# Kernel optimization log

Hardware: AMD Instinct MI355X
Metric: run time of the kernel (lower is better)

## Reference

```python
import jax, jax.numpy as jnp
import numpy as np
from functools import partial

T, B, IN, H = 512, 32, 1024, 1024
NUM_LAYERS = 2
SLOPE, OFFSET = 0.2, 0.5
FORGET_GATE_BIAS = 1.0
W_SCALE = 1.0 / np.sqrt(H)  # mimics reset_parameters uniform(-1/sqrt(H), 1/sqrt(H)) scale


def setup_inputs() -> dict:
    key = jax.random.key(0)
    ks = jax.random.split(key, 12)
    x = jax.random.normal(ks[0], (T, B, IN), dtype=jnp.float32)
    h0 = jax.random.normal(ks[1], (NUM_LAYERS, B, H), dtype=jnp.float32)
    c0 = jax.random.normal(ks[2], (NUM_LAYERS, B, H), dtype=jnp.float32)
    def u(k, shape):
        return jax.random.uniform(k, shape, jnp.float32, -W_SCALE, W_SCALE)
    # layer 0: input_size=IN, layer 1: input_size=H
    W_ih0 = u(ks[3], (4 * H, IN))
    W_hh0 = u(ks[4], (4 * H, H))
    b_ih0 = u(ks[5], (4 * H,)).at[H:2 * H].set(FORGET_GATE_BIAS)
    b_hh0 = u(ks[6], (4 * H,)).at[H:2 * H].set(0.0)
    W_ih1 = u(ks[7], (4 * H, H))
    W_hh1 = u(ks[8], (4 * H, H))
    b_ih1 = u(ks[9], (4 * H,)).at[H:2 * H].set(FORGET_GATE_BIAS)
    b_hh1 = u(ks[10], (4 * H,)).at[H:2 * H].set(0.0)
    return {"x": x, "h0": h0, "c0": c0,
            "W_ih0": W_ih0, "W_hh0": W_hh0, "b_ih0": b_ih0, "b_hh0": b_hh0,
            "W_ih1": W_ih1, "W_hh1": W_hh1, "b_ih1": b_ih1, "b_hh1": b_hh1}


def _hard_sigmoid(g):
    return jnp.clip(SLOPE * g + OFFSET, 0.0, 1.0)


def _hardtanh(g):
    return jnp.clip(g, -1.0, 1.0)


def _run_layer(x, h, c, W_ih, W_hh, b_ih, b_hh):
    """HardLSTMLayerForward: per-step eps = mean(x_t) is added to input and state."""
    def step(carry, xt):
        h, c = carry
        eps = jnp.mean(xt)
        xi = xt + eps          # [B, in]
        hh = h + eps           # [B, H]
        cc = c + eps           # [B, H]
        gates = xi @ W_ih.T + b_ih + hh @ W_hh.T + b_hh  # [B, 4H]
        i_g = _hard_sigmoid(gates[:, :H])
        f_g = _hard_sigmoid(gates[:, H:2 * H])
        g_g = _hardtanh(gates[:, 2 * H:3 * H])
        o_g = _hard_sigmoid(gates[:, 3 * H:])
        cy = f_g * cc + i_g * g_g
        hy = o_g * _hardtanh(cy)
        return (hy, cy), hy
    (h, c), y = jax.lax.scan(step, (h, c), x)
    return y, h, c


def reference(x, h0, c0, W_ih0, W_hh0, b_ih0, b_hh0, W_ih1, W_hh1, b_ih1, b_hh1):
    out = x + 1.0  # StackedLSTM adds `one` to the input
    y0, h_0, c_0 = _run_layer(out, h0[0], c0[0], W_ih0, W_hh0, b_ih0, b_hh0)
    y1, h_1, c_1 = _run_layer(y0, h0[1], c0[1], W_ih1, W_hh1, b_ih1, b_hh1)
    hn = jnp.stack([h_0, h_1])  # [num_layers, B, H]
    cn = jnp.stack([c_0, c_1])
    return (y1, hn, cn)
```

## Files before the change

### kernel.cpp

```cpp
#include <hip/hip_runtime.h>
#include <cstdio>


#define T_STEPS 512
#define DEADLINE_TICKS 6000000ULL

typedef __bf16 bf16x8 __attribute__((ext_vector_type(8)));
typedef float  f32x4  __attribute__((ext_vector_type(4)));
typedef unsigned int u32x4 __attribute__((ext_vector_type(4)));
typedef unsigned long long u64;

#define AGLD(p)   __hip_atomic_load((p), __ATOMIC_RELAXED, __HIP_MEMORY_SCOPE_AGENT)
#define AGST(p,v) __hip_atomic_store((p), (v), __ATOMIC_RELAXED, __HIP_MEMORY_SCOPE_AGENT)
#define MFMA16 __builtin_amdgcn_mfma_f32_16x16x32_bf16

__device__ __forceinline__ u64 rtick(){ return __builtin_amdgcn_s_memrealtime(); }

__device__ __forceinline__ unsigned short f2bf(float f){
  union { float f; unsigned u; } v; v.f = f;
  unsigned r = v.u + 0x7FFFu + ((v.u >> 16) & 1u);
  return (unsigned short)(r >> 16);
}
__device__ __forceinline__ bf16x8 packbf(f32x4 a, f32x4 b){
  unsigned u0 = f2bf(a[0]) | ((unsigned)f2bf(a[1])<<16);
  unsigned u1 = f2bf(a[2]) | ((unsigned)f2bf(a[3])<<16);
  unsigned u2 = f2bf(b[0]) | ((unsigned)f2bf(b[1])<<16);
  unsigned u3 = f2bf(b[2]) | ((unsigned)f2bf(b[3])<<16);
  u32x4 cv = {u0,u1,u2,u3};
  return __builtin_bit_cast(bf16x8, cv);
}
__device__ __forceinline__ int fragOff(int row, int k8){
  return ((k8>>2)*2 + (row>>4))*1024 + ((row&15) | ((k8&3)<<4))*16;
}
__device__ __forceinline__ bf16x8 ld_frag_plain(const char* p){
  u32x4 v = *reinterpret_cast<const u32x4*>(p);
  return __builtin_bit_cast(bf16x8, v);
}
__device__ __forceinline__ bf16x8 lds_frag(const char* p){
  u32x4 v = *reinterpret_cast<const u32x4*>(p);
  return __builtin_bit_cast(bf16x8, v);
}

__device__ __forceinline__ void stage64k(const char* src, char* dst, int tid){
  u32x4 r0,r1,r2,r3,r4,r5,r6,r7,r8,r9,ra,rb,rc,rd,re,rf;
  u64 a = (u64)(uintptr_t)src + (u64)tid*16;
  #define LD(reg, off) asm volatile("global_load_dwordx4 %0, %1, off sc0 sc1" \
                                    : "=v"(reg) : "v"(a + (off)) : "memory")
  LD(r0,0); LD(r1,4096); LD(r2,8192); LD(r3,12288);
  LD(r4,16384); LD(r5,20480); LD(r6,24576); LD(r7,28672);
  LD(r8,32768); LD(r9,36864); LD(ra,40960); LD(rb,45056);
  LD(rc,49152); LD(rd,53248); LD(re,57344); LD(rf,61440);
  #undef LD
  asm volatile("s_waitcnt vmcnt(0)" ::: "memory");
  u32x4* d = (u32x4*)(dst + tid*16);
  d[0]=r0; d[256]=r1; d[512]=r2; d[768]=r3;
  d[1024]=r4; d[1280]=r5; d[1536]=r6; d[1792]=r7;
  d[2048]=r8; d[2304]=r9; d[2560]=ra; d[2816]=rb;
  d[3072]=rc; d[3328]=rd; d[3584]=re; d[3840]=rf;
}

__device__ __forceinline__ void spin128(const unsigned short* f, unsigned tgt,
                                        int lane, u64 dl){
  if (lane < 16){
    u64 a = (u64)(uintptr_t)f + (u64)lane*16;
    while (true){
      u32x4 v;
      asm volatile("global_load_dwordx4 %0, %1, off sc0 sc1\n\ts_waitcnt vmcnt(0)"
                   : "=v"(v) : "v"(a) : "memory");
      bool ok = true;
      #pragma unroll
      for (int i=0;i<4;++i){
        unsigned u = v[i];
        ok = ok && ((u & 0xFFFFu) >= tgt) && ((u >> 16) >= tgt);
      }
      if (__all((int)ok)) break;
      if (rtick() > dl) break;
    }
  }
  asm volatile("" ::: "memory");
}


__global__ void prep_xfrag(const float* __restrict__ x, unsigned short* __restrict__ xf){
  int tid = blockIdx.x*256 + threadIdx.x;
  int k8 = tid & 127, row = (tid>>7)&31, t = tid>>12;
  const float* s = x + ((size_t)(t*32+row)*1024 + k8*8);
  f32x4 a = *reinterpret_cast<const f32x4*>(s);
  f32x4 b = *reinterpret_cast<const f32x4*>(s+4);
  f32x4 a1 = {a[0]+1.f,a[1]+1.f,a[2]+1.f,a[3]+1.f};
  f32x4 b1 = {b[0]+1.f,b[1]+1.f,b[2]+1.f,b[3]+1.f};
  bf16x8 v = packbf(a1,b1);
  *reinterpret_cast<bf16x8*>((char*)xf + (size_t)t*65536 + fragOff(row,k8)) = v;
}

__global__ void prep_hfrag(const float* __restrict__ h0, unsigned short* __restrict__ hf){
  int tid = blockIdx.x*256 + threadIdx.x;
  int k8 = tid & 127, row = (tid>>7)&31, L = tid>>12;
  const float* s = h0 + ((size_t)(L*32+row)*1024 + k8*8);
  f32x4 a = *reinterpret_cast<const f32x4*>(s);
  f32x4 b = *reinterpret_cast<const f32x4*>(s+4);
  bf16x8 v = packbf(a,b);
  *reinterpret_cast<bf16x8*>((char*)hf + (size_t)L*65536 + fragOff(row,k8)) = v;
}

__global__ void reduce_mean_f32(const float* __restrict__ src, float* __restrict__ out, float add){
  __shared__ float red[256];
  int t = blockIdx.x, tid = threadIdx.x;
  const float* p = src + (size_t)t*32768;
  float s = 0.f;
  for (int i = tid; i < 32768; i += 256) s += p[i];
  red[tid] = s; __syncthreads();
  for (int o = 128; o > 0; o >>= 1){ if (tid < o) red[tid] += red[tid+o]; __syncthreads(); }
  if (tid == 0) out[t] = red[0]*(1.f/32768.f) + add;
}

__global__ void prep_rs(const float* __restrict__ Wih0, const float* __restrict__ Whh0,
                        const float* __restrict__ Wih1, const float* __restrict__ Whh1,
                        const float* __restrict__ bih0, const float* __restrict__ bhh0,
                        const float* __restrict__ bih1, const float* __restrict__ bhh1,
                        float* __restrict__ rs, float* __restrict__ bias){
  int task = blockIdx.x*4 + (threadIdx.x >> 6);
  int lane = threadIdx.x & 63;
  int L = task >> 12, n = task & 4095;
  const float* pi = (L ? Wih1 : Wih0) + (size_t)n*1024;
  const float* ph = (L ? Whh1 : Whh0) + (size_t)n*1024;
  float s = 0.f;
  #pragma unroll
  for (int e = 0; e < 16; ++e){ int k = lane + e*64; s += pi[k] + ph[k]; }
  #pragma unroll
  for (int m = 32; m; m >>= 1) s += __shfl_xor(s, m);
  if (lane == 0){
    rs[task]   = s;
    bias[task] = (L ? bih1[n] : bih0[n]) + (L ? bhh1[n] : bhh0[n]);
  }
}

__global__ __launch_bounds__(256) void rec8(
    const unsigned short* __restrict__ Xf,
    const unsigned short* __restrict__ HiniF,
    unsigned short* __restrict__ Ring0,
    unsigned short* __restrict__ Ring1,
    float* __restrict__ out,
    const float* __restrict__ Wih0, const float* __restrict__ Whh0,
    const float* __restrict__ Wih1, const float* __restrict__ Whh1,
    const float* __restrict__ biasC, const float* __restrict__ rsC,
    const float* __restrict__ eps0, const float* __restrict__ c0,
    int* __restrict__ epsP,
    unsigned short* __restrict__ flag0,
    unsigned short* __restrict__ flag1)
{
  __shared__ char ldsW[65536];
  __shared__ char ldsA[65536];
  __shared__ float ldsPs[4];

  const int tid  = threadIdx.x;
  const int lane = tid & 63;
  const int w    = tid >> 6;
  const int L    = blockIdx.x >> 7;
  const int bid  = blockIdx.x & 127;
  const int rh   = w >> 1;
  const int cg   = w & 1;
  const int jb   = bid * 8;
  const int jc   = jb + cg*4;
  const int c    = lane & 15;
  const int q    = c >> 2;
  const int ncol = q*1024 + jc + (c & 3);
  const int koff = (lane >> 4) << 3;
  const u64 dl   = rtick() + DEADLINE_TICKS;

  const float* Wfirst = L ? Whh1 : Wih0;
  const float* Wsec   = L ? Wih1 : Whh0;

  for (int i = 0; i < 16; ++i){
    int fi = w*16 + i;
    int cgx = fi >> 5, kt = fi & 31;
    int nn = q*1024 + jb + cgx*4 + (c & 3);
    const float* src = Wfirst + (size_t)nn*1024 + kt*32 + koff;
    f32x4 wa = *reinterpret_cast<const f32x4*>(src);
    f32x4 wb = *reinterpret_cast<const f32x4*>(src + 4);
    *reinterpret_cast<bf16x8*>(ldsW + fi*1024 + lane*16) = packbf(wa, wb);
  }
  bf16x8 wreg[32];
  {
    const float* src = Wsec + (size_t)ncol*1024 + koff;
    #pragma unroll
    for (int kt = 0; kt < 32; ++kt){
      f32x4 wa = *reinterpret_cast<const f32x4*>(src + kt*32);
      f32x4 wb = *reinterpret_cast<const f32x4*>(src + kt*32 + 4);
      wreg[kt] = packbf(wa, wb);
    }
  }
  __syncthreads();

  const float bia = biasC[L*4096 + ncol];
  const float rsv = rsC[L*4096 + ncol];
  const int jw = jc + (c & 3);
  float creg[4];
  #pragma unroll
  for (int r = 0; r < 4; ++r)
    creg[r] = c0[L*32768 + (rh*16 + (lane>>4)*4 + r)*1024 + jw];

  float* outHn = out + 16777216 + L*32768;
  float* outCn = out + 16777216 + 65536 + L*32768;
  const u64 myFlagA = (u64)(uintptr_t)((L ? flag1 : flag0) + bid);

  for (int t = 0; t < T_STEPS; ++t){
    f32x4 acc = {0.f, 0.f, 0.f, 0.f};
    float et;

    if (L == 0){
      const char* Ax = (const char*)Xf + (size_t)t*65536;
      #pragma unroll 4
      for (int kt = 0; kt < 32; ++kt){
        bf16x8 a = ld_frag_plain(Ax + (kt*2 + rh)*1024 + lane*16);
        bf16x8 b = lds_frag(ldsW + (cg*32 + kt)*1024 + lane*16);
        acc = MFMA16(a, b, acc, 0, 0, 0);
      }
      et = eps0[t];
      if (w == 0 && t > 0) spin128(flag0, (unsigned)t, lane, dl);
      __syncthreads();
      const char* hsrc = (t == 0) ? (const char*)HiniF
                                  : (const char*)Ring0 + (size_t)(t-1)*65536;
      stage64k(hsrc, ldsA, tid);
      __syncthreads();
      #pragma unroll 4
      for (int kt = 0; kt < 32; ++kt){
        bf16x8 a = lds_frag(ldsA + (kt*2 + rh)*1024 + lane*16);
        acc = MFMA16(a, wreg[kt], acc, 0, 0, 0);
      }
    } else {
      if (w == 0 && t > 0) spin128(flag1, (unsigned)t, lane, dl);
      __syncthreads();
      const char* hsrc = (t == 0) ? (const char*)HiniF + 65536
                                  : (const char*)Ring1 + (size_t)((t-1)&7)*65536;
      stage64k(hsrc, ldsA, tid);
      __syncthreads();
      #pragma unroll 4
      for (int kt = 0; kt < 32; ++kt){
        bf16x8 a = lds_frag(ldsA + (kt*2 + rh)*1024 + lane*16);
        bf16x8 b = lds_frag(ldsW + (cg*32 + kt)*1024 + lane*16);
        acc = MFMA16(a, b, acc, 0, 0, 0);
      }
      __syncthreads();
      if (w == 0) spin128(flag0, (unsigned)(t+1), lane, dl);
      __syncthreads();
      {
        const u64* ep = reinterpret_cast<const u64*>(epsP + (size_t)t*128);
        u64 v = AGLD(ep + lane);
        int s = (int)(unsigned)v + (int)(unsigned)(v >> 32);
        #pragma unroll
        for (int mm = 32; mm; mm >>= 1) s += __shfl_xor(s, mm);
        et = (float)s * 4.6566128730773926e-10f;
      }
      stage64k((const char*)Ring0 + (size_t)t*65536, ldsA, tid);
      __syncthreads();
      #pragma unroll 4
      for (int kt = 0; kt < 32; ++kt){
        bf16x8 a = lds_frag(ldsA + (kt*2 + rh)*1024 + lane*16);
        acc = MFMA16(a, wreg[kt], acc, 0, 0, 0);
      }
    }

    char* ringSlot = L ? ((char*)Ring1 + (size_t)(t & 7)*65536)
                       : ((char*)Ring0 + (size_t)t*65536);
    float hyv[4];
    float psum = 0.f;
    #pragma unroll
    for (int r = 0; r < 4; ++r){
      float g  = acc[r] + bia + et*rsv;
      float p4 = __shfl_xor(g, 4), p8 = __shfl_xor(g, 8), p12 = __shfl_xor(p4, 8);
      float iv = (q==0)?g:(q==1)?p4:(q==2)?p8:p12;
      float fv = (q==1)?g:(q==0)?p4:(q==3)?p8:p12;
      float gv = (q==2)?g:(q==3)?p4:(q==0)?p8:p12;
      float ov = (q==3)?g:(q==2)?p4:(q==1)?p8:p12;
      iv = fminf(fmaxf(0.2f*iv + 0.5f, 0.f), 1.f);
      fv = fminf(fmaxf(0.2f*fv + 0.5f, 0.f), 1.f);
      gv = fminf(fmaxf(gv, -1.f), 1.f);
      ov = fminf(fmaxf(0.2f*ov + 0.5f, 0.f), 1.f);
      float cc = fv*(creg[r] + et) + iv*gv;
      creg[r] = cc;
      float hy = ov * fminf(fmaxf(cc, -1.f), 1.f);
      hyv[r] = hy;
      if (c < 4) psum += hy;

      unsigned short hu = f2bf(hy);
      unsigned p2 = (unsigned)hu | (((unsigned)__shfl_xor((int)hu, 1)) << 16);
      unsigned q2 = (unsigned)__shfl_xor((int)p2, 2);
      if (c == 0){
        int sub = (lane>>4)*4 + r;
        size_t bo = (size_t)((jb>>5)*2 + rh)*1024
                  + (size_t)(sub | (((jb>>3)&3)<<4))*16 + (size_t)cg*8;
        AGST(reinterpret_cast<u64*>(ringSlot + bo), (u64)p2 | ((u64)q2 << 32));
      }
    }
    if (L == 0){
      #pragma unroll
      for (int mm = 32; mm; mm >>= 1) psum += __shfl_xor(psum, mm);
      if (lane == 0) ldsPs[w] = psum;
    }
    asm volatile("s_waitcnt vmcnt(0)" ::: "memory");
    __syncthreads();
    if (tid == 0){
      if (L == 0){
        float bs = ldsPs[0] + ldsPs[1] + ldsPs[2] + ldsPs[3];
        AGST(reinterpret_cast<unsigned*>(epsP + (size_t)t*128 + bid),
             (unsigned)(int)llrintf(bs*65536.f));
        asm volatile("s_waitcnt vmcnt(0)" ::: "memory");
      }
      asm volatile("global_store_short %0, %1, off sc0 sc1"
                   :: "v"(myFlagA), "v"((unsigned)(t+1)) : "memory");
    }

    if (L){
      #pragma unroll
      for (int r = 0; r < 4; ++r){
        float hy = hyv[r];
        float f1 = __shfl_xor(hy, 1), f2 = __shfl_xor(hy, 2), f3 = __shfl_xor(f1, 2);
        if (c == 0){
          int row = rh*16 + (lane>>4)*4 + r;
          f32x4 o4 = {hy, f1, f2, f3};
          *reinterpret_cast<f32x4*>(out + (size_t)t*32768 + row*1024 + jc) = o4;
        }
      }
    }
    if (t == T_STEPS-1){
      #pragma unroll
      for (int r = 0; r < 4; ++r)
        if (c < 4){
          int row = rh*16 + (lane>>4)*4 + r;
          outHn[row*1024 + jw] = hyv[r];
          outCn[row*1024 + jw] = creg[r];
        }
    }
  }
}


extern "C" void kernel_launch(void* const* d_in, const int* in_sizes, int n_in,
                              void* d_out, int out_size, void* d_ws, size_t ws_size,
                              hipStream_t stream)
{
  const float* x    = (const float*)d_in[0];
  const float* h0   = (const float*)d_in[1];
  const float* c0   = (const float*)d_in[2];
  const float* Wih0 = (const float*)d_in[3];
  const float* Whh0 = (const float*)d_in[4];
  const float* bih0 = (const float*)d_in[5];
  const float* bhh0 = (const float*)d_in[6];
  const float* Wih1 = (const float*)d_in[7];
  const float* Whh1 = (const float*)d_in[8];
  const float* bih1 = (const float*)d_in[9];
  const float* bhh1 = (const float*)d_in[10];
  float* out = (float*)d_out;

  char* ws = (char*)d_ws;
  size_t off = 0;
  auto alloc = [&](size_t bytes)->char* {
    char* p = ws + off; off += (bytes + 255) & ~(size_t)255; return p;
  };
  unsigned short* Xf    = (unsigned short*)alloc((size_t)T_STEPS*65536);
  unsigned short* Ring0 = (unsigned short*)alloc((size_t)T_STEPS*65536);
  unsigned short* Ring1 = (unsigned short*)alloc((size_t)8*65536);
  unsigned short* HiniF = (unsigned short*)alloc(2*65536);
  float* eps0 = (float*)alloc(T_STEPS*4);
  float* bias = (float*)alloc(2*4096*4);
  float* rs   = (float*)alloc(2*4096*4);
  int*   epsP = (int*)alloc((size_t)T_STEPS*128*4);
  char* sync = alloc(1024);
  unsigned short* flag0 = (unsigned short*)sync;
  unsigned short* flag1 = (unsigned short*)(sync + 512);
  if (off > ws_size)
    fprintf(stderr, "HardLSTM: ws too small, need %zu have %zu\n", off, ws_size);

  hipMemsetAsync(sync, 0, 1024, stream);
  prep_xfrag<<<8192, 256, 0, stream>>>(x, Xf);
  prep_hfrag<<<32, 256, 0, stream>>>(h0, HiniF);
  reduce_mean_f32<<<T_STEPS, 256, 0, stream>>>(x, eps0, 1.0f);
  prep_rs<<<2048, 256, 0, stream>>>(Wih0, Whh0, Wih1, Whh1,
                                    bih0, bhh0, bih1, bhh1, rs, bias);

  rec8<<<256, 256, 0, stream>>>(Xf, HiniF, Ring0, Ring1, out,
      Wih0, Whh0, Wih1, Whh1, bias, rs, eps0, c0, epsP, flag0, flag1);
}
```

Baseline: 6.417 ms.

## Halve persistent blocks, keep both weight matrices in registers, widen per-wave tiles

The persistent recurrent kernel now runs on 128 blocks instead of 256. Each wave owns 4 gate-columns for all 32 batch rows and holds both bf16 weight slices in registers, so the LDS weight copy goes away. Fewer blocks means fewer flags to poll and fewer partial eps sums per step. Layer 1's ring buffer becomes a full per-step buffer when workspace allows, so its h-state loads can use ordinary cached loads instead of cache-bypassing ones. The trade-off is heavy register pressure (64 bf16x8 weight vectors per lane) and half as many CUs doing the per-step matmul.

```diff
diff --git a/kernel.cpp b/kernel.cpp
--- a/kernel.cpp
+++ b/kernel.cpp
@@ -41,7 +41,19 @@
   return __builtin_bit_cast(bf16x8, v);
 }
 
-__device__ __forceinline__ void stage64k(const char* src, char* dst, int tid){
+__device__ __forceinline__ void stage64k_c(const char* src, char* dst, int tid){
+  const u32x4* s = reinterpret_cast<const u32x4*>(src) + tid;
+  u32x4 r0 = s[0],    r1 = s[256],  r2 = s[512],  r3 = s[768];
+  u32x4 r4 = s[1024], r5 = s[1280], r6 = s[1536], r7 = s[1792];
+  u32x4 r8 = s[2048], r9 = s[2304], ra = s[2560], rb = s[2816];
+  u32x4 rc = s[3072], rd = s[3328], re = s[3584], rf = s[3840];
+  u32x4* d = (u32x4*)(dst + tid*16);
+  d[0]=r0; d[256]=r1; d[512]=r2; d[768]=r3;
+  d[1024]=r4; d[1280]=r5; d[1536]=r6; d[1792]=r7;
+  d[2048]=r8; d[2304]=r9; d[2560]=ra; d[2816]=rb;
+  d[3072]=rc; d[3328]=rd; d[3584]=re; d[3840]=rf;
+}
+__device__ __forceinline__ void stage64k_b(const char* src, char* dst, int tid){
   u32x4 r0,r1,r2,r3,r4,r5,r6,r7,r8,r9,ra,rb,rc,rd,re,rf;
   u64 a = (u64)(uintptr_t)src + (u64)tid*16;
   #define LD(reg, off) asm volatile("global_load_dwordx4 %0, %1, off sc0 sc1" \
@@ -59,9 +71,9 @@
   d[3072]=rc; d[3328]=rd; d[3584]=re; d[3840]=rf;
 }
 
-__device__ __forceinline__ void spin128(const unsigned short* f, unsigned tgt,
-                                        int lane, u64 dl){
-  if (lane < 16){
+__device__ __forceinline__ void spin64(const unsigned short* f, unsigned tgt,
+                                       int lane, u64 dl){
+  if (lane < 8){
     u64 a = (u64)(uintptr_t)f + (u64)lane*16;
     while (true){
       u32x4 v;
@@ -135,11 +147,12 @@
   }
 }
 
-__global__ __launch_bounds__(256) void rec8(
+__global__ __launch_bounds__(256, 1) void rec10(
     const unsigned short* __restrict__ Xf,
     const unsigned short* __restrict__ HiniF,
     unsigned short* __restrict__ Ring0,
     unsigned short* __restrict__ Ring1,
+    int ring1mask, int ring1cached,
     float* __restrict__ out,
     const float* __restrict__ Wih0, const float* __restrict__ Whh0,
     const float* __restrict__ Wih1, const float* __restrict__ Whh1,
@@ -149,148 +162,158 @@
     unsigned short* __restrict__ flag0,
     unsigned short* __restrict__ flag1)
 {
-  __shared__ char ldsW[65536];
   __shared__ char ldsA[65536];
   __shared__ float ldsPs[4];
 
   const int tid  = threadIdx.x;
   const int lane = tid & 63;
   const int w    = tid >> 6;
-  const int L    = blockIdx.x >> 7;
-  const int bid  = blockIdx.x & 127;
-  const int rh   = w >> 1;
-  const int cg   = w & 1;
-  const int jb   = bid * 8;
-  const int jc   = jb + cg*4;
+  const int L    = blockIdx.x >> 6;
+  const int bid  = blockIdx.x & 63;
+  const int jb   = bid * 16;
+  const int jc   = jb + w*4;
   const int c    = lane & 15;
   const int q    = c >> 2;
   const int ncol = q*1024 + jc + (c & 3);
   const int koff = (lane >> 4) << 3;
   const u64 dl   = rtick() + DEADLINE_TICKS;
 
+  __builtin_amdgcn_fence(__ATOMIC_ACQUIRE, "agent");
+  __syncthreads();
+
   const float* Wfirst = L ? Whh1 : Wih0;
   const float* Wsec   = L ? Wih1 : Whh0;
 
-  for (int i = 0; i < 16; ++i){
-    int fi = w*16 + i;
-    int cgx = fi >> 5, kt = fi & 31;
-    int nn = q*1024 + jb + cgx*4 + (c & 3);
-    const float* src = Wfirst + (size_t)nn*1024 + kt*32 + koff;
-    f32x4 wa = *reinterpret_cast<const f32x4*>(src);
-    f32x4 wb = *reinterpret_cast<const f32x4*>(src + 4);
-    *reinterpret_cast<bf16x8*>(ldsW + fi*1024 + lane*16) = packbf(wa, wb);
-  }
-  bf16x8 wreg[32];
+  bf16x8 wregF[32], wregS[32];
   {
-    const float* src = Wsec + (size_t)ncol*1024 + koff;
+    const float* sF = Wfirst + (size_t)ncol*1024 + koff;
+    const float* sS = Wsec   + (size_t)ncol*1024 + koff;
     #pragma unroll
     for (int kt = 0; kt < 32; ++kt){
-      f32x4 wa = *reinterpret_cast<const f32x4*>(src + kt*32);
-      f32x4 wb = *reinterpret_cast<const f32x4*>(src + kt*32 + 4);
-      wreg[kt] = packbf(wa, wb);
+      f32x4 a = *reinterpret_cast<const f32x4*>(sF + kt*32);
+      f32x4 b = *reinterpret_cast<const f32x4*>(sF + kt*32 + 4);
+      wregF[kt] = packbf(a, b);
+      f32x4 cc = *reinterpret_cast<const f32x4*>(sS + kt*32);
+      f32x4 d  = *reinterpret_cast<const f32x4*>(sS + kt*32 + 4);
+      wregS[kt] = packbf(cc, d);
     }
   }
-  __syncthreads();
 
   const float bia = biasC[L*4096 + ncol];
   const float rsv = rsC[L*4096 + ncol];
   const int jw = jc + (c & 3);
-  float creg[4];
+  float creg[2][4];
   #pragma unroll
-  for (int r = 0; r < 4; ++r)
-    creg[r] = c0[L*32768 + (rh*16 + (lane>>4)*4 + r)*1024 + jw];
+  for (int m = 0; m < 2; ++m)
+    #pragma unroll
+    for (int r = 0; r < 4; ++r)
+      creg[m][r] = c0[L*32768 + (m*16 + (lane>>4)*4 + r)*1024 + jw];
 
   float* outHn = out + 16777216 + L*32768;
   float* outCn = out + 16777216 + 65536 + L*32768;
   const u64 myFlagA = (u64)(uintptr_t)((L ? flag1 : flag0) + bid);
 
   for (int t = 0; t < T_STEPS; ++t){
-    f32x4 acc = {0.f, 0.f, 0.f, 0.f};
+    f32x4 acc0 = {0.f,0.f,0.f,0.f}, acc1 = {0.f,0.f,0.f,0.f};
     float et;
 
     if (L == 0){
       const char* Ax = (const char*)Xf + (size_t)t*65536;
       #pragma unroll 4
       for (int kt = 0; kt < 32; ++kt){
-        bf16x8 a = ld_frag_plain(Ax + (kt*2 + rh)*1024 + lane*16);
-        bf16x8 b = lds_frag(ldsW + (cg*32 + kt)*1024 + lane*16);
-        acc = MFMA16(a, b, acc, 0, 0, 0);
+        bf16x8 a0 = ld_frag_plain(Ax + (kt*2 + 0)*1024 + lane*16);
+        bf16x8 a1 = ld_frag_plain(Ax + (kt*2 + 1)*1024 + lane*16);
+        acc0 = MFMA16(a0, wregF[kt], acc0, 0, 0, 0);
+        acc1 = MFMA16(a1, wregF[kt], acc1, 0, 0, 0);
       }
       et = eps0[t];
-      if (w == 0 && t > 0) spin128(flag0, (unsigned)t, lane, dl);
+      if (w == 0 && t > 0) spin64(flag0, (unsigned)t, lane, dl);
       __syncthreads();
       const char* hsrc = (t == 0) ? (const char*)HiniF
                                   : (const char*)Ring0 + (size_t)(t-1)*65536;
-      stage64k(hsrc, ldsA, tid);
+      stage64k_c(hsrc, ldsA, tid);
       __syncthreads();
       #pragma unroll 4
       for (int kt = 0; kt < 32; ++kt){
-        bf16x8 a = lds_frag(ldsA + (kt*2 + rh)*1024 + lane*16);
-        acc = MFMA16(a, wreg[kt], acc, 0, 0, 0);
+        bf16x8 a0 = lds_frag(ldsA + (kt*2 + 0)*1024 + lane*16);
+        bf16x8 a1 = lds_frag(ldsA + (kt*2 + 1)*1024 + lane*16);
+        acc0 = MFMA16(a0, wregS[kt], acc0, 0, 0, 0);
+        acc1 = MFMA16(a1, wregS[kt], acc1, 0, 0, 0);
       }
     } else {
-      if (w == 0 && t > 0) spin128(flag1, (unsigned)t, lane, dl);
+      if (w == 0 && t > 0) spin64(flag1, (unsigned)t, lane, dl);
       __syncthreads();
       const char* hsrc = (t == 0) ? (const char*)HiniF + 65536
-                                  : (const char*)Ring1 + (size_t)((t-1)&7)*65536;
-      stage64k(hsrc, ldsA, tid);
+                                  : (const char*)Ring1 + (size_t)((t-1) & ring1mask)*65536;
+      if (t == 0 || ring1cached) stage64k_c(hsrc, ldsA, tid);
+      else                       stage64k_b(hsrc, ldsA, tid);
       __syncthreads();
       #pragma unroll 4
       for (int kt = 0; kt < 32; ++kt){
-        bf16x8 a = lds_frag(ldsA + (kt*2 + rh)*1024 + lane*16);
-        bf16x8 b = lds_frag(ldsW + (cg*32 + kt)*1024 + lane*16);
-        acc = MFMA16(a, b, acc, 0, 0, 0);
-      }
-      __syncthreads();
-      if (w == 0) spin128(flag0, (unsigned)(t+1), lane, dl);
+        bf16x8 a0 = lds_frag(ldsA + (kt*2 + 0)*1024 + lane*16);
+        bf16x8 a1 = lds_frag(ldsA + (kt*2 + 1)*1024 + lane*16);
+        acc0 = MFMA16(a0, wregF[kt], acc0, 0, 0, 0);
+        acc1 = MFMA16(a1, wregF[kt], acc1, 0, 0, 0);
+      }
+      __syncthreads();
+      if (w == 0) spin64(flag0, (unsigned)(t+1), lane, dl);
       __syncthreads();
       {
-        const u64* ep = reinterpret_cast<const u64*>(epsP + (size_t)t*128);
-        u64 v = AGLD(ep + lane);
-        int s = (int)(unsigned)v + (int)(unsigned)(v >> 32);
+        int s = 0;
+        const u64* ep = reinterpret_cast<const u64*>(epsP + (size_t)t*64);
+        if (lane < 32){
+          u64 v = AGLD(ep + lane);
+          s = (int)(unsigned)v + (int)(unsigned)(v >> 32);
+        }
         #pragma unroll
         for (int mm = 32; mm; mm >>= 1) s += __shfl_xor(s, mm);
         et = (float)s * 4.6566128730773926e-10f;
       }
-      stage64k((const char*)Ring0 + (size_t)t*65536, ldsA, tid);
+      stage64k_c((const char*)Ring0 + (size_t)t*65536, ldsA, tid);
       __syncthreads();
       #pragma unroll 4
       for (int kt = 0; kt < 32; ++kt){
-        bf16x8 a = lds_frag(ldsA + (kt*2 + rh)*1024 + lane*16);
-        acc = MFMA16(a, wreg[kt], acc, 0, 0, 0);
-      }
-    }
-
-    char* ringSlot = L ? ((char*)Ring1 + (size_t)(t & 7)*65536)
+        bf16x8 a0 = lds_frag(ldsA + (kt*2 + 0)*1024 + lane*16);
+        bf16x8 a1 = lds_frag(ldsA + (kt*2 + 1)*1024 + lane*16);
+        acc0 = MFMA16(a0, wregS[kt], acc0, 0, 0, 0);
+        acc1 = MFMA16(a1, wregS[kt], acc1, 0, 0, 0);
+      }
+    }
+
+    char* ringSlot = L ? ((char*)Ring1 + (size_t)(t & ring1mask)*65536)
                        : ((char*)Ring0 + (size_t)t*65536);
-    float hyv[4];
+    float hyv[2][4];
     float psum = 0.f;
     #pragma unroll
-    for (int r = 0; r < 4; ++r){
-      float g  = acc[r] + bia + et*rsv;
-      float p4 = __shfl_xor(g, 4), p8 = __shfl_xor(g, 8), p12 = __shfl_xor(p4, 8);
-      float iv = (q==0)?g:(q==1)?p4:(q==2)?p8:p12;
-      float fv = (q==1)?g:(q==0)?p4:(q==3)?p8:p12;
-      float gv = (q==2)?g:(q==3)?p4:(q==0)?p8:p12;
-      float ov = (q==3)?g:(q==2)?p4:(q==1)?p8:p12;
-      iv = fminf(fmaxf(0.2f*iv + 0.5f, 0.f), 1.f);
-      fv = fminf(fmaxf(0.2f*fv + 0.5f, 0.f), 1.f);
-      gv = fminf(fmaxf(gv, -1.f), 1.f);
-      ov = fminf(fmaxf(0.2f*ov + 0.5f, 0.f), 1.f);
-      float cc = fv*(creg[r] + et) + iv*gv;
-      creg[r] = cc;
-      float hy = ov * fminf(fmaxf(cc, -1.f), 1.f);
-      hyv[r] = hy;
-      if (c < 4) psum += hy;
-
-      unsigned short hu = f2bf(hy);
-      unsigned p2 = (unsigned)hu | (((unsigned)__shfl_xor((int)hu, 1)) << 16);
-      unsigned q2 = (unsigned)__shfl_xor((int)p2, 2);
-      if (c == 0){
-        int sub = (lane>>4)*4 + r;
-        size_t bo = (size_t)((jb>>5)*2 + rh)*1024
-                  + (size_t)(sub | (((jb>>3)&3)<<4))*16 + (size_t)cg*8;
-        AGST(reinterpret_cast<u64*>(ringSlot + bo), (u64)p2 | ((u64)q2 << 32));
+    for (int m = 0; m < 2; ++m){
+      f32x4 av = m ? acc1 : acc0;
+      #pragma unroll
+      for (int r = 0; r < 4; ++r){
+        float g  = av[r] + bia + et*rsv;
+        float p4 = __shfl_xor(g, 4), p8 = __shfl_xor(g, 8), p12 = __shfl_xor(p4, 8);
+        float iv = (q==0)?g:(q==1)?p4:(q==2)?p8:p12;
+        float fv = (q==1)?g:(q==0)?p4:(q==3)?p8:p12;
+        float gv = (q==2)?g:(q==3)?p4:(q==0)?p8:p12;
+        float ov = (q==3)?g:(q==2)?p4:(q==1)?p8:p12;
+        iv = fminf(fmaxf(0.2f*iv + 0.5f, 0.f), 1.f);
+        fv = fminf(fmaxf(0.2f*fv + 0.5f, 0.f), 1.f);
+        gv = fminf(fmaxf(gv, -1.f), 1.f);
+        ov = fminf(fmaxf(0.2f*ov + 0.5f, 0.f), 1.f);
+        float cc = fv*(creg[m][r] + et) + iv*gv;
+        creg[m][r] = cc;
+        float hy = ov * fminf(fmaxf(cc, -1.f), 1.f);
+        hyv[m][r] = hy;
+        if (c < 4) psum += hy;
+
+        unsigned short hu = f2bf(hy);
+        unsigned p2 = (unsigned)hu | (((unsigned)__shfl_xor((int)hu, 1)) << 16);
+        unsigned q2 = (unsigned)__shfl_xor((int)p2, 2);
+        if (c == 0){
+          int sub = (lane>>4)*4 + r;
+          size_t bo = (size_t)((jc>>5)*2 + m)*1024
+                    + (size_t)(sub | (((jc>>3)&3)<<4))*16 + (size_t)(jc&7)*2;
+          AGST(reinterpret_cast<u64*>(ringSlot + bo), (u64)p2 | ((u64)q2 << 32));
+        }
       }
     }
     if (L == 0){
@@ -303,7 +326,7 @@
     if (tid == 0){
       if (L == 0){
         float bs = ldsPs[0] + ldsPs[1] + ldsPs[2] + ldsPs[3];
-        AGST(reinterpret_cast<unsigned*>(epsP + (size_t)t*128 + bid),
+        AGST(reinterpret_cast<unsigned*>(epsP + (size_t)t*64 + bid),
              (unsigned)(int)llrintf(bs*65536.f));
         asm volatile("s_waitcnt vmcnt(0)" ::: "memory");
       }
@@ -313,24 +336,28 @@
 
     if (L){
       #pragma unroll
-      for (int r = 0; r < 4; ++r){
-        float hy = hyv[r];
-        float f1 = __shfl_xor(hy, 1), f2 = __shfl_xor(hy, 2), f3 = __shfl_xor(f1, 2);
-        if (c == 0){
-          int row = rh*16 + (lane>>4)*4 + r;
-          f32x4 o4 = {hy, f1, f2, f3};
-          *reinterpret_cast<f32x4*>(out + (size_t)t*32768 + row*1024 + jc) = o4;
+      for (int m = 0; m < 2; ++m)
+        #pragma unroll
+        for (int r = 0; r < 4; ++r){
+          float hy = hyv[m][r];
+          float f1 = __shfl_xor(hy, 1), f2 = __shfl_xor(hy, 2), f3 = __shfl_xor(f1, 2);
+          if (c == 0){
+            int row = m*16 + (lane>>4)*4 + r;
+            f32x4 o4 = {hy, f1, f2, f3};
+            *reinterpret_cast<f32x4*>(out + (size_t)t*32768 + row*1024 + jc) = o4;
+          }
         }
-      }
     }
     if (t == T_STEPS-1){
       #pragma unroll
-      for (int r = 0; r < 4; ++r)
-        if (c < 4){
-          int row = rh*16 + (lane>>4)*4 + r;
-          outHn[row*1024 + jw] = hyv[r];
-          outCn[row*1024 + jw] = creg[r];
-        }
+      for (int m = 0; m < 2; ++m)
+        #pragma unroll
+        for (int r = 0; r < 4; ++r)
+          if (c < 4){
+            int row = m*16 + (lane>>4)*4 + r;
+            outHn[row*1024 + jw] = hyv[m][r];
+            outCn[row*1024 + jw] = creg[m][r];
+          }
     }
   }
 }
@@ -360,25 +387,29 @@
   };
   unsigned short* Xf    = (unsigned short*)alloc((size_t)T_STEPS*65536);
   unsigned short* Ring0 = (unsigned short*)alloc((size_t)T_STEPS*65536);
-  unsigned short* Ring1 = (unsigned short*)alloc((size_t)8*65536);
   unsigned short* HiniF = (unsigned short*)alloc(2*65536);
   float* eps0 = (float*)alloc(T_STEPS*4);
   float* bias = (float*)alloc(2*4096*4);
   float* rs   = (float*)alloc(2*4096*4);
-  int*   epsP = (int*)alloc((size_t)T_STEPS*128*4);
-  char* sync = alloc(1024);
+  int*   epsP = (int*)alloc((size_t)T_STEPS*64*4);
+  char* sync  = alloc(512);
   unsigned short* flag0 = (unsigned short*)sync;
-  unsigned short* flag1 = (unsigned short*)(sync + 512);
+  unsigned short* flag1 = (unsigned short*)(sync + 128);
+  size_t remain  = (off <= ws_size) ? (ws_size - off) : 0;
+  int r1slots    = (remain >= (size_t)(T_STEPS+1)*65536) ? T_STEPS : 8;
+  unsigned short* Ring1 = (unsigned short*)alloc((size_t)r1slots*65536);
+  int r1mask   = r1slots - 1;
+  int r1cached = (r1slots == T_STEPS) ? 1 : 0;
   if (off > ws_size)
     fprintf(stderr, "HardLSTM: ws too small, need %zu have %zu\n", off, ws_size);
 
-  hipMemsetAsync(sync, 0, 1024, stream);
+  hipMemsetAsync(sync, 0, 512, stream);
   prep_xfrag<<<8192, 256, 0, stream>>>(x, Xf);
   prep_hfrag<<<32, 256, 0, stream>>>(h0, HiniF);
   reduce_mean_f32<<<T_STEPS, 256, 0, stream>>>(x, eps0, 1.0f);
   prep_rs<<<2048, 256, 0, stream>>>(Wih0, Whh0, Wih1, Whh1,
                                     bih0, bhh0, bih1, bhh1, rs, bias);
 
-  rec8<<<256, 256, 0, stream>>>(Xf, HiniF, Ring0, Ring1, out,
+  rec10<<<128, 256, 0, stream>>>(Xf, HiniF, Ring0, Ring1, r1mask, r1cached, out,
       Wih0, Whh0, Wih1, Whh1, bias, rs, eps0, c0, epsP, flag0, flag1);
 }
```

Measured after the change: 7.598 ms. 18.4% more time.
